# Performance work log

Measured on AMD Instinct MI355X. Metric: run time of the kernel, lower is better.

## Reference

```python
import jax, jax.numpy as jnp
import numpy as np

B, NH, T, N, D = 4, 8, 2048, 512, 128
THETA = 2.0 ** 16
GAMMA = 0.995


def setup_inputs() -> dict:
    key = jax.random.key(0)
    kq, kv, ks = jax.random.split(key, 3)
    Q = jax.random.normal(kq, (B, NH, T, N), jnp.float32)
    V = jax.random.normal(kv, (B, NH, T, D), jnp.float32)
    S_prev = 0.01 * jax.random.normal(ks, (B, NH, N, D), jnp.float32)
    # get_freqs(N, theta=2**16): per-channel inverse frequencies
    freqs = jnp.asarray(1.0 / THETA ** (np.arange(N, dtype=np.float32) / N), jnp.float32)
    gamma = jnp.float32(GAMMA)
    return {"Q": Q, "V": V, "S_prev": S_prev, "freqs": freqs, "gamma": gamma}


def _rope(phases, v):
    """Rotary embedding with per-channel phases. phases broadcasts against v's
    last two dims (T, N); rotate-half formulation."""
    cos, sin = jnp.cos(phases), jnp.sin(phases)
    half = v.shape[-1] // 2
    v_rot = jnp.concatenate([-v[..., half:], v[..., :half]], axis=-1)
    return v * cos + v_rot * sin


def reference(Q, V, S_prev, freqs, gamma):
    # Q: (B,nh,T,N)  V: (B,nh,T,D)  S_prev: (B,nh,N,D)
    t_len = Q.shape[2]
    phases = jnp.arange(t_len, dtype=freqs.dtype)[:, None] * freqs[None, :]  # (T,N)
    QR = _rope(phases[None, None], Q)  # K == Q per the module's assert

    q_seq = jnp.moveaxis(QR, 2, 0)  # (T,B,nh,N)
    v_seq = jnp.moveaxis(V, 2, 0)   # (T,B,nh,D)

    def step(S, qv):
        q_t, v_t = qv
        out_t = jnp.einsum('bhn,bhnd->bhd', q_t, S)          # read before write
        S_new = (S + jnp.einsum('bhn,bhd->bhnd', q_t, v_t)) * gamma  # write + decay
        return S_new, out_t

    S_final, outs = jax.lax.scan(step, S_prev, (q_seq, v_seq))
    output = jnp.moveaxis(outs, 0, 2)  # (B,nh,T,D)
    return output, S_final
```

## Files before the change

kernel.cpp:

```cpp
#include <hip/hip_runtime.h>
#include <hip/hip_bf16.h>

typedef __attribute__((ext_vector_type(8))) short short8;
typedef __attribute__((ext_vector_type(4))) float f32x4;

#define MFMA16(a,b,c) __builtin_amdgcn_mfma_f32_16x16x32_bf16((a),(b),(c),0,0,0)

constexpr int BHn = 32;
constexpr int Tn  = 2048;
constexpr int Nn  = 512;
constexpr int Dn  = 128;
constexpr int CHn = 64;
constexpr int NCH = Tn / CHn;

static __device__ __forceinline__ unsigned short f2b(float x){
  __hip_bfloat16 h = __float2bfloat16(x);
  return *reinterpret_cast<unsigned short*>(&h);
}

__global__ __launch_bounds__(256) void rope_k(const float* __restrict__ Q,
                                              const float* __restrict__ freqs,
                                              unsigned short* __restrict__ QR){
  int gid = blockIdx.x * 256 + threadIdx.x;
  int np  = gid & 255;
  int t   = gid >> 8;
  float tf = (float)t;
  float f1 = freqs[np], f2 = freqs[np + 256];
  float s1, c1, s2, c2;
  sincosf(tf * f1, &s1, &c1);
  sincosf(tf * f2, &s2, &c2);
  size_t off = (size_t)t * Nn + np;
  for (int bh = 0; bh < BHn; ++bh){
    size_t base = (size_t)bh * Tn * Nn + off;
    float q1 = Q[base], q2 = Q[base + 256];
    QR[base]       = f2b(q1 * c1 - q2 * s1);
    QR[base + 256] = f2b(q2 * c2 + q1 * s2);
  }
}

__device__ __forceinline__ short8 ldfrag(const unsigned short* buf, int rowbase, int k0, int ld, int lane){
  int row = rowbase + (lane & 15);
  int col = (k0 + ((lane >> 4) << 3)) ^ ((row & 7) << 3);
  return *reinterpret_cast<const short8*>(buf + row * ld + col);
}

__device__ __forceinline__ void stage_Rs(unsigned short* Rs, uint4 a, uint4 b, int dt, int n0){
  *reinterpret_cast<uint4*>(&Rs[ dt      * 512 + (n0 ^ (( dt      & 7) << 3))]) = a;
  *reinterpret_cast<uint4*>(&Rs[(dt + 1) * 512 + (n0 ^ (((dt + 1) & 7) << 3))]) = b;
}

__global__ __launch_bounds__(512, 1) void lattn_main(
    const unsigned short* __restrict__ QR,
    const float* __restrict__ V,
    const float* __restrict__ S_prev,
    const float* __restrict__ gammap,
    float* __restrict__ Out,
    float* __restrict__ Sfin)
{
  __shared__ __align__(16) unsigned short Rs [64 * 512];
  __shared__ __align__(16) unsigned short SbTs[16 * 512];
  __shared__ __align__(16) unsigned short VTs[2][16 * 64];
  __shared__ __align__(16) unsigned short Ps [64 * 64];
  __shared__ float gpow[65], gpinv[65];

  const int tid  = threadIdx.x;
  const int w    = tid >> 6;
  const int lane = tid & 63;
  const int bh   = blockIdx.x & 31;
  const int dch  = blockIdx.x >> 5;
  const int d0   = dch * 16;
  const float g  = gammap[0];

  const unsigned short* QRbh = QR + (size_t)bh * Tn * Nn;
  const float* Vbh = V + (size_t)bh * Tn * Dn;

  if (tid < 65){
    gpow[tid]  = powf(g,  (float)tid);
    gpinv[tid] = powf(g, -(float)tid);
  }
  #pragma unroll
  for (int i = tid; i < 64 * 64; i += 512) Ps[i] = 0;

  f32x4 st[8];
  if (w >= 4){
    int r0 = (w - 4) * 8;
    #pragma unroll
    for (int j = 0; j < 8; ++j){
      int n = (r0 + j) * 16 + (lane & 15);
      const float* sp = S_prev + (size_t)bh * Nn * Dn + (size_t)n * Dn + d0 + ((lane >> 4) << 2);
      st[j] = *reinterpret_cast<const f32x4*>(sp);
    }
  }
  __syncthreads();
  const float g64 = gpow[64];

  {
    #pragma unroll
    for (int i = 0; i < 4; ++i){
      int p  = tid + i * 512;
      int dt = (p >> 6) << 1;
      int n0 = (p & 63) << 3;
      const unsigned short* src = QRbh + (size_t)dt * Nn + n0;
      uint4 a = *reinterpret_cast<const uint4*>(src);
      uint4 b = *reinterpret_cast<const uint4*>(src + Nn);
      stage_Rs(Rs, a, b, dt, n0);
    }
    {
      int dtv = tid >> 3, dp = (tid & 7) << 1;
      const float* vp = Vbh + (size_t)dtv * Dn + d0 + dp;
      float sc = gpinv[dtv];
      VTs[0][ dp      * 64 + (dtv ^ (( dp      & 7) << 3))] = f2b(vp[0] * sc);
      VTs[0][(dp + 1) * 64 + (dtv ^ (((dp + 1) & 7) << 3))] = f2b(vp[1] * sc);
    }
    if (w >= 4){
      int r0 = (w - 4) * 8;
      #pragma unroll
      for (int j = 0; j < 8; ++j){
        int n  = (r0 + j) * 16 + (lane & 15);
        int dl = (lane >> 4) << 2;
        #pragma unroll
        for (int r = 0; r < 4; ++r){
          int d = dl + r;
          SbTs[d * 512 + (n ^ ((d & 7) << 3))] = f2b(st[j][r]);
        }
      }
    }
  }
  __syncthreads();

  for (int c = 0; c < NCH; ++c){
    const int t0 = c * CHn;
    const int vb = c & 1;
    const bool pf = (c + 1 < NCH);
    const unsigned short* Qc = QRbh + (size_t)t0 * Nn;

    uint4 ra[4], rb[4];
    float va0 = 0.f, va1 = 0.f;
    const int n0_  = (tid & 63) << 3;
    const int dtv_ = tid >> 3;
    if (pf){
      const unsigned short* QRc = QRbh + (size_t)(t0 + CHn) * Nn;
      #pragma unroll
      for (int i = 0; i < 4; ++i){
        int dt = (((tid >> 6) + 8 * i) << 1);
        const unsigned short* src = QRc + (size_t)dt * Nn + n0_;
        ra[i] = *reinterpret_cast<const uint4*>(src);
        rb[i] = *reinterpret_cast<const uint4*>(src + Nn);
      }
      const float* vp = Vbh + (size_t)(t0 + CHn + dtv_) * Dn + d0 + ((tid & 7) << 1);
      va0 = vp[0]; va1 = vp[1];
    }

    f32x4 oacc = {0.f, 0.f, 0.f, 0.f};
    if (w < 4){
      f32x4 p0 = {0.f,0.f,0.f,0.f}, p1 = p0, p2 = p0;
      for (int kb = 0; kb < 16; ++kb){
        int k0 = kb * 32;
        short8 fs = ldfrag(SbTs, 0, k0, 512, lane);
        if (w == 0){
          short8 f0 = ldfrag(Rs,  0, k0, 512, lane);
          short8 f1 = ldfrag(Rs, 16, k0, 512, lane);
          p0   = MFMA16(f0, f0, p0);
          p1   = MFMA16(f1, f0, p1);
          p2   = MFMA16(f1, f1, p2);
          oacc = MFMA16(fs, f0, oacc);
        } else if (w == 1){
          short8 f0 = ldfrag(Rs,  0, k0, 512, lane);
          short8 f1 = ldfrag(Rs, 16, k0, 512, lane);
          short8 f2 = ldfrag(Rs, 32, k0, 512, lane);
          p0   = MFMA16(f2, f0, p0);
          p1   = MFMA16(f2, f1, p1);
          p2   = MFMA16(f2, f2, p2);
          oacc = MFMA16(fs, f2, oacc);
        } else if (w == 2){
          short8 f0 = ldfrag(Rs,  0, k0, 512, lane);
          short8 f1 = ldfrag(Rs, 16, k0, 512, lane);
          short8 f3 = ldfrag(Rs, 48, k0, 512, lane);
          p0   = MFMA16(f3, f0, p0);
          p1   = MFMA16(f3, f1, p1);
          oacc = MFMA16(fs, f3, oacc);
        } else {
          short8 f1 = ldfrag(Rs, 16, k0, 512, lane);
          short8 f2 = ldfrag(Rs, 32, k0, 512, lane);
          short8 f3 = ldfrag(Rs, 48, k0, 512, lane);
          p0   = MFMA16(f3, f2, p0);
          p1   = MFMA16(f3, f3, p1);
          oacc = MFMA16(fs, f1, oacc);
        }
      }
      int tI[3], tJ[3], nt;
      if      (w == 0){ tI[0]=0; tJ[0]=0; tI[1]=1; tJ[1]=0; tI[2]=1; tJ[2]=1; nt = 3; }
      else if (w == 1){ tI[0]=2; tJ[0]=0; tI[1]=2; tJ[1]=1; tI[2]=2; tJ[2]=2; nt = 3; }
      else if (w == 2){ tI[0]=3; tJ[0]=0; tI[1]=3; tJ[1]=1; tI[2]=0; tJ[2]=0; nt = 2; }
      else            { tI[0]=3; tJ[0]=2; tI[1]=3; tJ[1]=3; tI[2]=0; tJ[2]=0; nt = 2; }
      f32x4 pacc[3] = {p0, p1, p2};
      for (int q = 0; q < nt; ++q){
        int j  = tJ[q] * 16 + (lane & 15);
        int i0 = tI[q] * 16 + ((lane >> 4) << 2);
        #pragma unroll
        for (int r = 0; r < 4; ++r){
          int i = i0 + r;
          float v = (j < i) ? pacc[q][r] * gpow[i] : 0.f;
          Ps[i * 64 + (j ^ ((i & 7) << 3))] = f2b(v);
        }
      }
    } else {
      int r0 = (w - 4) * 8;
      #pragma unroll
      for (int ks = 0; ks < 2; ++ks){
        short8 av = ldfrag(VTs[vb], 0, ks * 32, 64, lane);
        #pragma unroll
        for (int j = 0; j < 8; ++j){
          int n = (r0 + j) * 16 + (lane & 15);
          const unsigned short* col = Qc + (size_t)(ks * 32 + ((lane >> 4) << 3)) * Nn + n;
          short8 bn;
          #pragma unroll
          for (int e = 0; e < 8; ++e) bn[e] = (short)col[(size_t)e * Nn];
          st[j] = MFMA16(av, bn, st[j]);
        }
      }
      #pragma unroll
      for (int j = 0; j < 8; ++j)
        #pragma unroll
        for (int r = 0; r < 4; ++r) st[j][r] *= g64;
    }
    __syncthreads();

    if (w >= 4){
      int r0 = (w - 4) * 8;
      #pragma unroll
      for (int j = 0; j < 8; ++j){
        int n  = (r0 + j) * 16 + (lane & 15);
        int dl = (lane >> 4) << 2;
        #pragma unroll
        for (int r = 0; r < 4; ++r){
          int d = dl + r;
          SbTs[d * 512 + (n ^ ((d & 7) << 3))] = f2b(st[j][r]);
        }
      }
    } else {
      const int itl = (w == 0) ? 0 : (w == 1) ? 2 : (w == 2) ? 3 : 1;
      float gi = gpow[itl * 16 + (lane & 15)];
      #pragma unroll
      for (int r = 0; r < 4; ++r) oacc[r] *= gi;
      #pragma unroll
      for (int ks = 0; ks < 2; ++ks){
        short8 av = ldfrag(VTs[vb], 0, ks * 32, 64, lane);
        short8 bp = ldfrag(Ps, itl * 16, ks * 32, 64, lane);
        oacc = MFMA16(av, bp, oacc);
      }
      int ti = t0 + itl * 16 + (lane & 15);
      float* op = Out + (size_t)bh * Tn * Dn + (size_t)ti * Dn + d0 + ((lane >> 4) << 2);
      *reinterpret_cast<f32x4*>(op) = oacc;
    }
    if (pf){
      #pragma unroll
      for (int i = 0; i < 4; ++i){
        int dt = (((tid >> 6) + 8 * i) << 1);
        stage_Rs(Rs, ra[i], rb[i], dt, n0_);
      }
      int dp = (tid & 7) << 1;
      float sc = gpinv[dtv_];
      VTs[vb ^ 1][ dp      * 64 + (dtv_ ^ (( dp      & 7) << 3))] = f2b(va0 * sc);
      VTs[vb ^ 1][(dp + 1) * 64 + (dtv_ ^ (((dp + 1) & 7) << 3))] = f2b(va1 * sc);
    }
    __syncthreads();
  }

  if (w >= 4){
    int r0 = (w - 4) * 8;
    #pragma unroll
    for (int j = 0; j < 8; ++j){
      int n = (r0 + j) * 16 + (lane & 15);
      float* sp = Sfin + (size_t)bh * Nn * Dn + (size_t)n * Dn + d0 + ((lane >> 4) << 2);
      *reinterpret_cast<f32x4*>(sp) = st[j];
    }
  }
}

extern "C" void kernel_launch(void* const* d_in, const int* in_sizes, int n_in,
                              void* d_out, int out_size, void* d_ws, size_t ws_size,
                              hipStream_t stream){
  const float* Q      = (const float*)d_in[0];
  const float* V      = (const float*)d_in[1];
  const float* S_prev = (const float*)d_in[2];
  const float* freqs  = (const float*)d_in[3];
  const float* gamma  = (const float*)d_in[4];
  float* Out  = (float*)d_out;
  float* Sfin = Out + (size_t)BHn * Tn * Dn;
  unsigned short* QR = (unsigned short*)d_ws;

  rope_k<<<2048, 256, 0, stream>>>(Q, freqs, QR);
  lattn_main<<<256, 512, 0, stream>>>(QR, V, S_prev, gamma, Out, Sfin);
}
```

Measured before the change: 202.0 us.

## Store rotated Q in time-quad interleaved layout for vectorized column loads

The RoPE kernel now writes QR with groups of four consecutive timesteps interleaved per channel, and each block handles 4 timesteps for 8 heads so the sincos results are reused. The main kernel's state-update path previously gathered eight strided scalar bf16 loads per MFMA operand; it now issues two 8-byte vector loads. Staging into shared memory de-interleaves the quads with bit shuffles and 32-bit stores. The trade-off is more ALU work and narrower LDS stores during staging.

```diff
diff --git a/kernel.cpp b/kernel.cpp
--- a/kernel.cpp
+++ b/kernel.cpp
@@ -2,6 +2,7 @@
 #include <hip/hip_bf16.h>
 
 typedef __attribute__((ext_vector_type(8))) short short8;
+typedef __attribute__((ext_vector_type(4))) short short4v;
 typedef __attribute__((ext_vector_type(4))) float f32x4;
 
 #define MFMA16(a,b,c) __builtin_amdgcn_mfma_f32_16x16x32_bf16((a),(b),(c),0,0,0)
@@ -20,21 +21,31 @@
 
 __global__ __launch_bounds__(256) void rope_k(const float* __restrict__ Q,
                                               const float* __restrict__ freqs,
-                                              unsigned short* __restrict__ QR){
-  int gid = blockIdx.x * 256 + threadIdx.x;
-  int np  = gid & 255;
-  int t   = gid >> 8;
-  float tf = (float)t;
+                                              unsigned short* __restrict__ QRq){
+  int tq  = blockIdx.x & 511;
+  int bh0 = (blockIdx.x >> 9) << 3;
+  int np  = threadIdx.x;
   float f1 = freqs[np], f2 = freqs[np + 256];
-  float s1, c1, s2, c2;
-  sincosf(tf * f1, &s1, &c1);
-  sincosf(tf * f2, &s2, &c2);
-  size_t off = (size_t)t * Nn + np;
-  for (int bh = 0; bh < BHn; ++bh){
-    size_t base = (size_t)bh * Tn * Nn + off;
-    float q1 = Q[base], q2 = Q[base + 256];
-    QR[base]       = f2b(q1 * c1 - q2 * s1);
-    QR[base + 256] = f2b(q2 * c2 + q1 * s2);
+  float s1[4], c1[4], s2[4], c2[4];
+  #pragma unroll
+  for (int i = 0; i < 4; ++i){
+    float tf = (float)(tq * 4 + i);
+    sincosf(tf * f1, &s1[i], &c1[i]);
+    sincosf(tf * f2, &s2[i], &c2[i]);
+  }
+  for (int b = 0; b < 8; ++b){
+    int bh = bh0 + b;
+    const float* qp = Q + (size_t)bh * Tn * Nn + (size_t)(tq * 4) * Nn + np;
+    short4v o1, o2;
+    #pragma unroll
+    for (int i = 0; i < 4; ++i){
+      float q1 = qp[(size_t)i * Nn], q2 = qp[(size_t)i * Nn + 256];
+      o1[i] = (short)f2b(q1 * c1[i] - q2 * s1[i]);
+      o2[i] = (short)f2b(q2 * c2[i] + q1 * s2[i]);
+    }
+    unsigned short* dst = QRq + (size_t)bh * Tn * Nn + (size_t)tq * 2048;
+    *reinterpret_cast<short4v*>(dst + np * 4)         = o1;
+    *reinterpret_cast<short4v*>(dst + (np + 256) * 4) = o2;
   }
 }
 
@@ -44,13 +55,20 @@
   return *reinterpret_cast<const short8*>(buf + row * ld + col);
 }
 
-__device__ __forceinline__ void stage_Rs(unsigned short* Rs, uint4 a, uint4 b, int dt, int n0){
-  *reinterpret_cast<uint4*>(&Rs[ dt      * 512 + (n0 ^ (( dt      & 7) << 3))]) = a;
-  *reinterpret_cast<uint4*>(&Rs[(dt + 1) * 512 + (n0 ^ (((dt + 1) & 7) << 3))]) = b;
+__device__ __forceinline__ void stage_q(unsigned short* Rs, uint4 v, int dt0, int n0){
+  unsigned w0 = v.x, w1 = v.y, w2 = v.z, w3 = v.w;
+  unsigned o0 = (w0 & 0xffffu) | (w2 << 16);
+  unsigned o1 = (w0 >> 16)     | (w2 & 0xffff0000u);
+  unsigned o2 = (w1 & 0xffffu) | (w3 << 16);
+  unsigned o3 = (w1 >> 16)     | (w3 & 0xffff0000u);
+  *reinterpret_cast<unsigned*>(&Rs[(dt0    ) * 512 + (n0 ^ (((dt0    ) & 7) << 3))]) = o0;
+  *reinterpret_cast<unsigned*>(&Rs[(dt0 + 1) * 512 + (n0 ^ (((dt0 + 1) & 7) << 3))]) = o1;
+  *reinterpret_cast<unsigned*>(&Rs[(dt0 + 2) * 512 + (n0 ^ (((dt0 + 2) & 7) << 3))]) = o2;
+  *reinterpret_cast<unsigned*>(&Rs[(dt0 + 3) * 512 + (n0 ^ (((dt0 + 3) & 7) << 3))]) = o3;
 }
 
 __global__ __launch_bounds__(512, 1) void lattn_main(
-    const unsigned short* __restrict__ QR,
+    const unsigned short* __restrict__ QRq,
     const float* __restrict__ V,
     const float* __restrict__ S_prev,
     const float* __restrict__ gammap,
@@ -71,7 +89,7 @@
   const int d0   = dch * 16;
   const float g  = gammap[0];
 
-  const unsigned short* QRbh = QR + (size_t)bh * Tn * Nn;
+  const unsigned short* QRbh = QRq + (size_t)bh * Tn * Nn;
   const float* Vbh = V + (size_t)bh * Tn * Dn;
 
   if (tid < 65){
@@ -96,14 +114,11 @@
 
   {
     #pragma unroll
-    for (int i = 0; i < 4; ++i){
-      int p  = tid + i * 512;
-      int dt = (p >> 6) << 1;
-      int n0 = (p & 63) << 3;
-      const unsigned short* src = QRbh + (size_t)dt * Nn + n0;
-      uint4 a = *reinterpret_cast<const uint4*>(src);
-      uint4 b = *reinterpret_cast<const uint4*>(src + Nn);
-      stage_Rs(Rs, a, b, dt, n0);
+    for (int i = 0; i < 8; ++i){
+      int p = tid + i * 512;
+      int tql = p >> 8, n0 = (p & 255) << 1;
+      uint4 v = *reinterpret_cast<const uint4*>(QRbh + (size_t)tql * 2048 + n0 * 4);
+      stage_q(Rs, v, tql << 2, n0);
     }
     {
       int dtv = tid >> 3, dp = (tid & 7) << 1;
@@ -134,18 +149,16 @@
     const bool pf = (c + 1 < NCH);
     const unsigned short* Qc = QRbh + (size_t)t0 * Nn;
 
-    uint4 ra[4], rb[4];
+    uint4 rq[8];
     float va0 = 0.f, va1 = 0.f;
-    const int n0_  = (tid & 63) << 3;
     const int dtv_ = tid >> 3;
     if (pf){
       const unsigned short* QRc = QRbh + (size_t)(t0 + CHn) * Nn;
       #pragma unroll
-      for (int i = 0; i < 4; ++i){
-        int dt = (((tid >> 6) + 8 * i) << 1);
-        const unsigned short* src = QRc + (size_t)dt * Nn + n0_;
-        ra[i] = *reinterpret_cast<const uint4*>(src);
-        rb[i] = *reinterpret_cast<const uint4*>(src + Nn);
+      for (int i = 0; i < 8; ++i){
+        int p = tid + i * 512;
+        int tql = p >> 8, n0 = (p & 255) << 1;
+        rq[i] = *reinterpret_cast<const uint4*>(QRc + (size_t)tql * 2048 + n0 * 4);
       }
       const float* vp = Vbh + (size_t)(t0 + CHn + dtv_) * Dn + d0 + ((tid & 7) << 1);
       va0 = vp[0]; va1 = vp[1];
@@ -211,11 +224,12 @@
         short8 av = ldfrag(VTs[vb], 0, ks * 32, 64, lane);
         #pragma unroll
         for (int j = 0; j < 8; ++j){
-          int n = (r0 + j) * 16 + (lane & 15);
-          const unsigned short* col = Qc + (size_t)(ks * 32 + ((lane >> 4) << 3)) * Nn + n;
-          short8 bn;
-          #pragma unroll
-          for (int e = 0; e < 8; ++e) bn[e] = (short)col[(size_t)e * Nn];
+          int n   = (r0 + j) * 16 + (lane & 15);
+          int dt0 = ks * 32 + ((lane >> 4) << 3);
+          const unsigned short* bp = Qc + (size_t)(dt0 >> 2) * 2048 + n * 4;
+          short4v lo = *reinterpret_cast<const short4v*>(bp);
+          short4v hi = *reinterpret_cast<const short4v*>(bp + 2048);
+          short8 bn = __builtin_shufflevector(lo, hi, 0, 1, 2, 3, 4, 5, 6, 7);
           st[j] = MFMA16(av, bn, st[j]);
         }
       }
@@ -255,9 +269,10 @@
     }
     if (pf){
       #pragma unroll
-      for (int i = 0; i < 4; ++i){
-        int dt = (((tid >> 6) + 8 * i) << 1);
-        stage_Rs(Rs, ra[i], rb[i], dt, n0_);
+      for (int i = 0; i < 8; ++i){
+        int p = tid + i * 512;
+        int tql = p >> 8, n0 = (p & 255) << 1;
+        stage_q(Rs, rq[i], tql << 2, n0);
       }
       int dp = (tid & 7) << 1;
       float sc = gpinv[dtv_];
@@ -288,8 +303,8 @@
   const float* gamma  = (const float*)d_in[4];
   float* Out  = (float*)d_out;
   float* Sfin = Out + (size_t)BHn * Tn * Dn;
-  unsigned short* QR = (unsigned short*)d_ws;
-
-  rope_k<<<2048, 256, 0, stream>>>(Q, freqs, QR);
-  lattn_main<<<256, 512, 0, stream>>>(QR, V, S_prev, gamma, Out, Sfin);
-}
+  unsigned short* QRq = (unsigned short*)d_ws;
+
+  rope_k<<<2048, 256, 0, stream>>>(Q, freqs, QRq);
+  lattn_main<<<256, 512, 0, stream>>>(QRq, V, S_prev, gamma, Out, Sfin);
+}
```

New measurement: 203.2 us. Within noise of the previous version (+0.6%).
